# Kernel optimization log

Hardware: AMD Instinct MI355X
Metric: run time of the kernel (lower is better)

Reference implementation:

```python
import jax, jax.numpy as jnp
import numpy as np

N, D = 256, 512
DIST_W, ANGLE_W = 1.0, 2.0
EPS_PD = 1e-6    # F.pairwise_distance eps (added to the difference)
EPS_COS = 1e-8   # F.cosine_similarity eps (denominator floor)
CLAMP = 1e-7     # acos clamp margin


def _smooth_l1(x):
    # F.smooth_l1_loss with beta=1.0, elementwise (reduction handled by caller)
    ax = jnp.abs(x)
    return jnp.where(ax < 1.0, 0.5 * ax * ax, ax - 0.5)


def _pairwise_dist(E):
    # Faithful to the looped version: dist[i,j] = ||e_i - e_j + eps|| for i<j,
    # mirrored to the lower triangle, zero diagonal.
    diff = E[:, None, :] - E[None, :, :] + EPS_PD          # [n, n, d]
    d = jnp.sqrt(jnp.sum(diff * diff, axis=-1))            # [n, n]
    upper = jnp.triu(d, k=1)
    return upper + upper.T


def _angles(E):
    # ang[j, i, k] = angle at vertex j between (e_i - e_j) and (e_k - e_j)
    Dv = E[None, :, :] - E[:, None, :]                     # Dv[j, a] = e_a - e_j
    norms = jnp.sqrt(jnp.sum(Dv * Dv, axis=-1))            # [n, n]
    dots = jnp.einsum('jad,jbd->jab', Dv, Dv)              # [n, n, n]
    denom = jnp.maximum(norms[:, :, None] * norms[:, None, :], EPS_COS)
    cos = jnp.clip(dots / denom, -1.0 + CLAMP, 1.0 - CLAMP)
    return jnp.arccos(cos)


def setup_inputs() -> dict:
    key = jax.random.key(0)
    k1, k2 = jax.random.split(key)
    return {
        'student_embeddings': jax.random.normal(k1, (N, D), dtype=jnp.float32),
        'teacher_embeddings': jax.random.normal(k2, (N, D), dtype=jnp.float32),
    }


def reference(student_embeddings, teacher_embeddings):
    # distance-wise loss: smooth_l1 mean over the full n x n matrix
    ds = _pairwise_dist(student_embeddings)
    dt = _pairwise_dist(teacher_embeddings)
    distance_loss = jnp.mean(_smooth_l1(ds - dt))

    # angle-wise loss: mean over triplets i<j<k (vertex at j)
    n = student_embeddings.shape[0]
    ang_s = _angles(student_embeddings)
    ang_t = _angles(teacher_embeddings)
    idx = jnp.arange(n)
    # mask[j, i, k] = (i < j) & (j < k)
    mask = (idx[None, :, None] < idx[:, None, None]) & (idx[:, None, None] < idx[None, None, :])
    count = n * (n - 1) * (n - 2) // 6
    angle_loss = jnp.sum(_smooth_l1(ang_s - ang_t) * mask) / count

    total_loss = DIST_W * distance_loss + ANGLE_W * angle_loss
    return (total_loss, distance_loss, angle_loss)
```

## Files before the change

kernel.cpp:

```cpp
#include <hip/hip_runtime.h>
#include <math.h>

#define N 256
#define D 512
#define SPLIT 4

using f32x4  = __attribute__((ext_vector_type(4))) float;
using bf16x8 = __attribute__((ext_vector_type(8))) short;

__device__ __forceinline__ short f2bf(float f) {
    unsigned u = __float_as_uint(f);
    u += 0x7fffu + ((u >> 16) & 1u);
    return (short)(u >> 16);
}

__device__ __forceinline__ float smooth_l1(float x) {
    float ax = fabsf(x);
    return ax < 1.f ? 0.5f * ax * ax : ax - 0.5f;
}

__device__ __forceinline__ float acos_fast(float x) {
    float ax = fabsf(x);
    float p = -0.0187293f;
    p = p * ax + 0.0742610f;
    p = p * ax - 0.2121144f;
    p = p * ax + 1.5707288f;
    float v = sqrtf(1.f - ax) * p;
    return x < 0.f ? 3.14159265358979f - v : v;
}

__global__ __launch_bounds__(64) void gram_kernel(const float* __restrict__ Es,
                                                  const float* __restrict__ Et,
                                                  float2* __restrict__ G2,
                                                  float* __restrict__ acc) {
    const int lane = threadIdx.x;
    if (blockIdx.x == 0 && blockIdx.y == 0 && blockIdx.z == 0 && lane == 0) {
        acc[0] = 0.f;
        acc[1] = 0.f;
    }
    const float* E = blockIdx.z ? Et : Es;
    const int m = lane & 15, quad = lane >> 4;
    const int baseA = (blockIdx.y * 16 + m) * D + quad * 8;
    const int baseB = (blockIdx.x * 16 + m) * D + quad * 8;

    f32x4 c = {0.f, 0.f, 0.f, 0.f};
#pragma unroll
    for (int k0 = 0; k0 < D; k0 += 32) {
        float4 alo = *(const float4*)&E[baseA + k0];
        float4 ahi = *(const float4*)&E[baseA + k0 + 4];
        float4 blo = *(const float4*)&E[baseB + k0];
        float4 bhi = *(const float4*)&E[baseB + k0 + 4];
        bf16x8 a, b;
        a[0] = f2bf(alo.x); a[1] = f2bf(alo.y); a[2] = f2bf(alo.z); a[3] = f2bf(alo.w);
        a[4] = f2bf(ahi.x); a[5] = f2bf(ahi.y); a[6] = f2bf(ahi.z); a[7] = f2bf(ahi.w);
        b[0] = f2bf(blo.x); b[1] = f2bf(blo.y); b[2] = f2bf(blo.z); b[3] = f2bf(blo.w);
        b[4] = f2bf(bhi.x); b[5] = f2bf(bhi.y); b[6] = f2bf(bhi.z); b[7] = f2bf(bhi.w);
        c = __builtin_amdgcn_mfma_f32_16x16x32_bf16(a, b, c, 0, 0, 0);
    }

    const int col = blockIdx.x * 16 + m;
#pragma unroll
    for (int r = 0; r < 4; ++r) {
        const int row = blockIdx.y * 16 + quad * 4 + r;
        ((float*)&G2[row * N + col])[blockIdx.z] = c[r];
    }
}

__global__ __launch_bounds__(256) void angle_dist_kernel(const float2* __restrict__ G2,
                                                         float* __restrict__ acc) {
    const int j = blockIdx.x + 1;
    const int tid = threadIdx.x;
    __shared__ float2 sv[N], tv[N];
    __shared__ float2 red[256];
    const float2 gjj = G2[j * N + j];
    const float Gsjj = gjj.x, Gtjj = gjj.y;

    float distp = 0.f;
    {
        const int a = tid;
        float2 gaj = G2[a * N + j];
        float2 gaa = G2[a * N + a];
        float n2s = gaa.x - 2.f * gaj.x + Gsjj;
        float n2t = gaa.y - 2.f * gaj.y + Gtjj;
        float rs = (a == j) ? 0.f : rsqrtf(n2s);
        float rt = (a == j) ? 0.f : rsqrtf(n2t);
        sv[a] = make_float2(gaj.x, rs);
        tv[a] = make_float2(gaj.y, rt);
        if (blockIdx.y == 0 && a < j)
            distp = smooth_l1(n2s * rs - n2t * rt);
    }
    __syncthreads();

    const int nk = 255 - j;
    const int npairs = j * nk;
    const float inv_nk = 1.0f / (float)nk;
    const float lo = -0.99999994f;
    const float hi = 0.99999994f;

    float anglep = 0.f;
    for (int p = blockIdx.y * 256 + tid; p < npairs; p += 256 * SPLIT) {
        int i = (int)((float)p * inv_nk);
        int rem = p - i * nk;
        if (rem < 0) { --i; rem += nk; }
        else if (rem >= nk) { ++i; rem -= nk; }
        const int k = j + 1 + rem;
        float2 si = sv[i], sk = sv[k];
        float2 ti = tv[i], tk = tv[k];
        float2 gik = G2[i * N + k];
        float dots = gik.x - si.x - sk.x + Gsjj;
        float dott = gik.y - ti.x - tk.x + Gtjj;
        float coss = fminf(fmaxf(dots * (si.y * sk.y), lo), hi);
        float cost = fminf(fmaxf(dott * (ti.y * tk.y), lo), hi);
        anglep += smooth_l1(acos_fast(coss) - acos_fast(cost));
    }

    red[tid] = make_float2(distp, anglep);
    __syncthreads();
    for (int s = 128; s > 0; s >>= 1) {
        if (tid < s) {
            red[tid].x += red[tid + s].x;
            red[tid].y += red[tid + s].y;
        }
        __syncthreads();
    }
    if (tid == 0) {
        atomicAdd(&acc[1], red[0].y);
        if (blockIdx.y == 0) atomicAdd(&acc[0], red[0].x);
    }
}

__global__ void finalize_kernel(const float* __restrict__ acc,
                                float* __restrict__ out) {
    float dl = 2.f * acc[0] / (float)(N * N);
    float al = acc[1] / (float)(N * (N - 1) * (N - 2) / 6);
    out[0] = 1.0f * dl + 2.0f * al;
    out[1] = dl;
    out[2] = al;
}

extern "C" void kernel_launch(void* const* d_in, const int* in_sizes, int n_in,
                              void* d_out, int out_size, void* d_ws, size_t ws_size,
                              hipStream_t stream) {
    const float* Es = (const float*)d_in[0];
    const float* Et = (const float*)d_in[1];
    float* out = (float*)d_out;
    float* ws = (float*)d_ws;

    float* acc = ws;
    float2* G2 = (float2*)(ws + 64);

    gram_kernel<<<dim3(16, 16, 2), 64, 0, stream>>>(Es, Et, G2, acc);
    angle_dist_kernel<<<dim3(N - 1, SPLIT), 256, 0, stream>>>(G2, acc);
    finalize_kernel<<<1, 1, 0, stream>>>(acc, out);
}
```

Baseline: 86.61 us.

## Compute symmetric Gram half, pack shared vectors, use wave-shuffle reduction

```diff
diff --git a/kernel.cpp b/kernel.cpp
--- a/kernel.cpp
+++ b/kernel.cpp
@@ -9,9 +9,8 @@
 using bf16x8 = __attribute__((ext_vector_type(8))) short;
 
 __device__ __forceinline__ short f2bf(float f) {
-    unsigned u = __float_as_uint(f);
-    u += 0x7fffu + ((u >> 16) & 1u);
-    return (short)(u >> 16);
+    __bf16 h = (__bf16)f;
+    return __builtin_bit_cast(short, h);
 }
 
 __device__ __forceinline__ float smooth_l1(float x) {
@@ -38,6 +37,8 @@
         acc[0] = 0.f;
         acc[1] = 0.f;
     }
+    if (blockIdx.y > blockIdx.x) return;
+
     const float* E = blockIdx.z ? Et : Es;
     const int m = lane & 15, quad = lane >> 4;
     const int baseA = (blockIdx.y * 16 + m) * D + quad * 8;
@@ -59,10 +60,13 @@
     }
 
     const int col = blockIdx.x * 16 + m;
+    const bool mirror = blockIdx.y < blockIdx.x;
 #pragma unroll
     for (int r = 0; r < 4; ++r) {
         const int row = blockIdx.y * 16 + quad * 4 + r;
         ((float*)&G2[row * N + col])[blockIdx.z] = c[r];
+        if (mirror)
+            ((float*)&G2[col * N + row])[blockIdx.z] = c[r];
     }
 }
 
@@ -70,8 +74,8 @@
                                                          float* __restrict__ acc) {
     const int j = blockIdx.x + 1;
     const int tid = threadIdx.x;
-    __shared__ float2 sv[N], tv[N];
-    __shared__ float2 red[256];
+    __shared__ float4 stv[N];
+    __shared__ float2 red[4];
     const float2 gjj = G2[j * N + j];
     const float Gsjj = gjj.x, Gtjj = gjj.y;
 
@@ -84,8 +88,7 @@
         float n2t = gaa.y - 2.f * gaj.y + Gtjj;
         float rs = (a == j) ? 0.f : rsqrtf(n2s);
         float rt = (a == j) ? 0.f : rsqrtf(n2t);
-        sv[a] = make_float2(gaj.x, rs);
-        tv[a] = make_float2(gaj.y, rt);
+        stv[a] = make_float4(gaj.x, rs, gaj.y, rt);
         if (blockIdx.y == 0 && a < j)
             distp = smooth_l1(n2s * rs - n2t * rt);
     }
@@ -104,28 +107,28 @@
         if (rem < 0) { --i; rem += nk; }
         else if (rem >= nk) { ++i; rem -= nk; }
         const int k = j + 1 + rem;
-        float2 si = sv[i], sk = sv[k];
-        float2 ti = tv[i], tk = tv[k];
+        float4 si = stv[i], sk = stv[k];
         float2 gik = G2[i * N + k];
         float dots = gik.x - si.x - sk.x + Gsjj;
-        float dott = gik.y - ti.x - tk.x + Gtjj;
+        float dott = gik.y - si.z - sk.z + Gtjj;
         float coss = fminf(fmaxf(dots * (si.y * sk.y), lo), hi);
-        float cost = fminf(fmaxf(dott * (ti.y * tk.y), lo), hi);
+        float cost = fminf(fmaxf(dott * (si.w * sk.w), lo), hi);
         anglep += smooth_l1(acos_fast(coss) - acos_fast(cost));
     }
 
-    red[tid] = make_float2(distp, anglep);
+    float vx = distp, vy = anglep;
+#pragma unroll
+    for (int off = 32; off > 0; off >>= 1) {
+        vx += __shfl_down(vx, off);
+        vy += __shfl_down(vy, off);
+    }
+    if ((tid & 63) == 0) red[tid >> 6] = make_float2(vx, vy);
     __syncthreads();
-    for (int s = 128; s > 0; s >>= 1) {
-        if (tid < s) {
-            red[tid].x += red[tid + s].x;
-            red[tid].y += red[tid + s].y;
-        }
-        __syncthreads();
-    }
     if (tid == 0) {
-        atomicAdd(&acc[1], red[0].y);
-        if (blockIdx.y == 0) atomicAdd(&acc[0], red[0].x);
+        float rx = red[0].x + red[1].x + red[2].x + red[3].x;
+        float ry = red[0].y + red[1].y + red[2].y + red[3].y;
+        atomicAdd(&acc[1], ry);
+        if (blockIdx.y == 0) atomicAdd(&acc[0], rx);
     }
 }
 
```

Result: faster. 84.77 us (-2.1%).
